# Kernel optimization log

Measured on AMD Instinct MI355X. Metric: run time of the kernel, lower is better.

## Reference

```python
import jax, jax.numpy as jnp
import numpy as np

B, H, S, D = 2, 16, 2048, 64


def setup_inputs() -> dict:
    key = jax.random.key(0)
    k1, k2, k3 = jax.random.split(key, 3)
    qry = jax.random.normal(k1, (B, H, S, D), dtype=jnp.float32)
    k_ = jax.random.normal(k2, (B, H, S, D), dtype=jnp.float32)
    val = jax.random.normal(k3, (B, H, S, D), dtype=jnp.float32)
    # causal mask [B, S_q, S_k]: True = attend, False = masked
    attn_mask = jnp.broadcast_to(jnp.tril(jnp.ones((S, S), dtype=bool)), (B, S, S))
    return {"qry": qry, "key": k_, "val": val, "attn_mask": attn_mask}


def reference(qry, key, val, attn_mask):
    d_k = key.shape[-1]
    # scores: [B, H, S_q, S_k]
    scores = jnp.einsum("bhqd,bhkd->bhqk", qry, key) / jnp.sqrt(jnp.asarray(d_k, qry.dtype))
    if attn_mask is not None:
        # attn_bias: 0 where mask True, -inf where False; broadcast over heads
        bias = jnp.where(attn_mask[:, None, :, :], jnp.asarray(0.0, qry.dtype), jnp.asarray(-jnp.inf, qry.dtype))
        scores = scores + bias
    attn_weights = jax.nn.softmax(scores, axis=-1)
    # dropout_p = 0.0 -> no dropout applied
    output = jnp.einsum("bhqk,bhkd->bhqd", attn_weights, val)
    return (output, attn_weights)
```

## Files before the change

### kernel.cpp

```cpp
#include <hip/hip_runtime.h>

#define NB 2
#define NH 16
#define SEQ 2048
#define HD 64

typedef __attribute__((ext_vector_type(8))) __bf16 bfrag8;
typedef __attribute__((ext_vector_type(4))) __bf16 bvec4;
typedef __attribute__((ext_vector_type(4))) float ffrag4;

#define SCALE2 0.18033688011112042f
#define MASKVAL (-3.0e38f)

__device__ __forceinline__ ffrag4 mfma16(bfrag8 a, bfrag8 b, ffrag4 c) {
    return __builtin_amdgcn_mfma_f32_16x16x32_bf16(a, b, c, 0, 0, 0);
}

__global__ __launch_bounds__(256, 4)
void attn_fwd(const float* __restrict__ Qg, const float* __restrict__ Kg,
              const float* __restrict__ Vg, float* __restrict__ Og,
              float* __restrict__ Pg)
{
    const int bh   = blockIdx.y;
    const int qt   = (blockIdx.x + blockIdx.y) & 31;
    const int q0   = qt * 64;
    const int tid  = threadIdx.x;
    const int wave = tid >> 6;
    const int lane = tid & 63;
    const int l16  = lane & 15;
    const int quad = lane >> 4;

    const float* Qb = Qg + (size_t)bh * SEQ * HD;
    const float* Kb = Kg + (size_t)bh * SEQ * HD;
    const float* Vb = Vg + (size_t)bh * SEQ * HD;
    float* Ob = Og + (size_t)bh * SEQ * HD;
    float* Pb = Pg + (size_t)bh * SEQ * SEQ;

    __shared__ __align__(16) char smem[35840];
    __bf16* Ks  = (__bf16*)smem;
    __bf16* Vts = (__bf16*)(smem + 9216);
    float*  P32 = (float*)(smem + 18432);
    __bf16* Qs  = (__bf16*)(smem + 18432);
    float*  Pw  = P32 + wave * (16 * 68);

    {
        const float4 z4 = make_float4(0.f, 0.f, 0.f, 0.f);
        for (int r = 0; r < 64; ++r) {
            float* dst = Pb + (size_t)(q0 + r) * SEQ;
            for (int c = q0 + 64 + tid * 4; c < SEQ; c += 1024)
                *(float4*)(dst + c) = z4;
        }
    }

    #pragma unroll
    for (int j = 0; j < 4; ++j) {
        int i = tid + 256 * j;
        int row = i >> 4, c4 = (i & 15) * 4;
        float4 v = *(const float4*)(Qb + (size_t)(q0 + row) * HD + c4);
        bvec4 w = { (__bf16)v.x, (__bf16)v.y, (__bf16)v.z, (__bf16)v.w };
        *(bvec4*)&Qs[row * 72 + c4] = w;
    }
    __syncthreads();
    bfrag8 qf0 = *(bfrag8*)&Qs[(wave * 16 + l16) * 72 +  0 + quad * 8];
    bfrag8 qf1 = *(bfrag8*)&Qs[(wave * 16 + l16) * 72 + 32 + quad * 8];

    const int nch   = q0 / 64 + 1;
    const int wrow  = q0 + wave * 16;
    const int myrow = wrow + quad * 4;

    float m_i[4], l_i[4], rl[4];
    #pragma unroll
    for (int r = 0; r < 4; ++r) { m_i[r] = MASKVAL; l_i[r] = 0.f; }

    for (int ch = 0; ch < nch; ++ch) {
        __syncthreads();
        #pragma unroll
        for (int j = 0; j < 4; ++j) {
            int i = tid + 256 * j;
            int row = i >> 4, c4 = (i & 15) * 4;
            float4 v = *(const float4*)(Kb + (size_t)(ch * 64 + row) * HD + c4);
            bvec4 w = { (__bf16)v.x, (__bf16)v.y, (__bf16)v.z, (__bf16)v.w };
            *(bvec4*)&Ks[row * 72 + c4] = w;
        }
        __syncthreads();

        ffrag4 acc[4] = { {0,0,0,0},{0,0,0,0},{0,0,0,0},{0,0,0,0} };
        #pragma unroll
        for (int g = 0; g < 4; ++g) {
            bfrag8 b0 = *(bfrag8*)&Ks[(g * 16 + l16) * 72 + quad * 8];
            bfrag8 b1 = *(bfrag8*)&Ks[(g * 16 + l16) * 72 + 32 + quad * 8];
            acc[g] = mfma16(qf0, b0, acc[g]);
            acc[g] = mfma16(qf1, b1, acc[g]);
        }
        #pragma unroll
        for (int r = 0; r < 4; ++r) {
            const int row = myrow + r;
            float s0 = (ch * 64 +  0 + l16 <= row) ? acc[0][r] * SCALE2 : MASKVAL;
            float s1 = (ch * 64 + 16 + l16 <= row) ? acc[1][r] * SCALE2 : MASKVAL;
            float s2 = (ch * 64 + 32 + l16 <= row) ? acc[2][r] * SCALE2 : MASKVAL;
            float s3 = (ch * 64 + 48 + l16 <= row) ? acc[3][r] * SCALE2 : MASKVAL;
            float mn = fmaxf(fmaxf(s0, s1), fmaxf(s2, s3));
            mn = fmaxf(mn, m_i[r]);
            float e = exp2f(s0 - mn) + exp2f(s1 - mn)
                    + exp2f(s2 - mn) + exp2f(s3 - mn);
            l_i[r] = l_i[r] * exp2f(m_i[r] - mn) + e;
            m_i[r] = mn;
        }
    }

    #pragma unroll
    for (int r = 0; r < 4; ++r) {
        float m = m_i[r], l = l_i[r];
        #pragma unroll
        for (int d = 1; d < 16; d <<= 1) {
            float om = __shfl_xor(m, d, 16);
            float ol = __shfl_xor(l, d, 16);
            float mn = fmaxf(m, om);
            l = l * exp2f(m - mn) + ol * exp2f(om - mn);
            m = mn;
        }
        m_i[r] = m;
        rl[r]  = 1.f / l;
    }

    ffrag4 oacc[4] = { {0,0,0,0},{0,0,0,0},{0,0,0,0},{0,0,0,0} };
    for (int ch = 0; ch < nch; ++ch) {
        __syncthreads();
        #pragma unroll
        for (int j = 0; j < 4; ++j) {
            int i = tid + 256 * j;
            int row = i >> 4, c4 = (i & 15) * 4;
            float4 v = *(const float4*)(Kb + (size_t)(ch * 64 + row) * HD + c4);
            bvec4 w = { (__bf16)v.x, (__bf16)v.y, (__bf16)v.z, (__bf16)v.w };
            *(bvec4*)&Ks[row * 72 + c4] = w;
        }
        #pragma unroll
        for (int j = 0; j < 4; ++j) {
            int i = tid + 256 * j;
            int kk = i >> 4, c4 = (i & 15) * 4;
            float4 v = *(const float4*)(Vb + (size_t)(ch * 64 + kk) * HD + c4);
            Vts[(c4 + 0) * 72 + kk] = (__bf16)v.x;
            Vts[(c4 + 1) * 72 + kk] = (__bf16)v.y;
            Vts[(c4 + 2) * 72 + kk] = (__bf16)v.z;
            Vts[(c4 + 3) * 72 + kk] = (__bf16)v.w;
        }
        __syncthreads();

        ffrag4 acc[4] = { {0,0,0,0},{0,0,0,0},{0,0,0,0},{0,0,0,0} };
        #pragma unroll
        for (int g = 0; g < 4; ++g) {
            bfrag8 b0 = *(bfrag8*)&Ks[(g * 16 + l16) * 72 + quad * 8];
            bfrag8 b1 = *(bfrag8*)&Ks[(g * 16 + l16) * 72 + 32 + quad * 8];
            acc[g] = mfma16(qf0, b0, acc[g]);
            acc[g] = mfma16(qf1, b1, acc[g]);
        }
        #pragma unroll
        for (int r = 0; r < 4; ++r) {
            const int row = myrow + r;
            #pragma unroll
            for (int g = 0; g < 4; ++g) {
                int col = ch * 64 + g * 16 + l16;
                float p = (col <= row)
                        ? exp2f(acc[g][r] * SCALE2 - m_i[r]) * rl[r] : 0.f;
                Pw[(quad * 4 + r) * 68 + g * 16 + l16] = p;
            }
        }
        asm volatile("s_waitcnt lgkmcnt(0)" ::: "memory");

        #pragma unroll
        for (int t = 0; t < 4; ++t) {
            int row = (lane >> 4) + t * 4;
            float4 v = *(float4*)&Pw[row * 68 + (lane & 15) * 4];
            *(float4*)(Pb + (size_t)(wrow + row) * SEQ + ch * 64 + (lane & 15) * 4) = v;
        }

        #pragma unroll
        for (int h = 0; h < 2; ++h) {
            float4 p0 = *(float4*)&Pw[l16 * 68 + h * 32 + quad * 8];
            float4 p1 = *(float4*)&Pw[l16 * 68 + h * 32 + quad * 8 + 4];
            bfrag8 pa = { (__bf16)p0.x, (__bf16)p0.y, (__bf16)p0.z, (__bf16)p0.w,
                          (__bf16)p1.x, (__bf16)p1.y, (__bf16)p1.z, (__bf16)p1.w };
            #pragma unroll
            for (int t = 0; t < 4; ++t) {
                bfrag8 bv = *(bfrag8*)&Vts[(t * 16 + l16) * 72 + h * 32 + quad * 8];
                oacc[t] = mfma16(pa, bv, oacc[t]);
            }
        }
    }

    #pragma unroll
    for (int t = 0; t < 4; ++t)
        #pragma unroll
        for (int r = 0; r < 4; ++r)
            Ob[(size_t)(myrow + r) * HD + t * 16 + l16] = oacc[t][r];
}

extern "C" void kernel_launch(void* const* d_in, const int* in_sizes, int n_in,
                              void* d_out, int out_size, void* d_ws, size_t ws_size,
                              hipStream_t stream) {
    const float* Qg = (const float*)d_in[0];
    const float* Kg = (const float*)d_in[1];
    const float* Vg = (const float*)d_in[2];
    float* Og = (float*)d_out;
    float* Pg = Og + (size_t)NB * NH * SEQ * HD;
    dim3 grid(SEQ / 64, NB * NH);
    attn_fwd<<<grid, dim3(256), 0, stream>>>(Qg, Kg, Vg, Og, Pg);
}
```

Measured before the change: 714.9 us.

## Pre-convert K and transposed V to bf16 workspace and use nontemporal P stores

Adds a pre-pass kernel that converts K to bf16 and V to a transposed bf16 layout in workspace once per call. The attention kernel then loads half the bytes per tile and skips repeated fp32-to-bf16 conversion and scattered transposing LDS writes across its two passes. Stores of the large attention-weights matrix, including the zero fill, become nontemporal to reduce cache pollution. The cost is an extra kernel launch and a workspace round trip.

```diff
diff --git a/kernel.cpp b/kernel.cpp
--- a/kernel.cpp
+++ b/kernel.cpp
@@ -8,6 +8,7 @@
 typedef __attribute__((ext_vector_type(8))) __bf16 bfrag8;
 typedef __attribute__((ext_vector_type(4))) __bf16 bvec4;
 typedef __attribute__((ext_vector_type(4))) float ffrag4;
+typedef __attribute__((ext_vector_type(4))) float f32x4;
 
 #define SCALE2 0.18033688011112042f
 #define MASKVAL (-3.0e38f)
@@ -16,9 +17,52 @@
     return __builtin_amdgcn_mfma_f32_16x16x32_bf16(a, b, c, 0, 0, 0);
 }
 
+__global__ __launch_bounds__(256)
+void cvt_kv(const float* __restrict__ Kg, const float* __restrict__ Vg,
+            __bf16* __restrict__ Kw, __bf16* __restrict__ Vtw)
+{
+    const int bh = blockIdx.y;
+    const int t0 = blockIdx.x * 64;
+    const int tid = threadIdx.x;
+
+    const float* Kb = Kg + (size_t)bh * SEQ * HD;
+    const float* Vb = Vg + (size_t)bh * SEQ * HD;
+    __bf16* Kwb = Kw  + (size_t)bh * SEQ * HD;
+    __bf16* Vwb = Vtw + (size_t)bh * SEQ * HD;
+
+    #pragma unroll
+    for (int j = 0; j < 4; ++j) {
+        int i = tid + 256 * j;
+        int row = i >> 4, c4 = (i & 15) * 4;
+        float4 v = *(const float4*)(Kb + (size_t)(t0 + row) * HD + c4);
+        bvec4 w = { (__bf16)v.x, (__bf16)v.y, (__bf16)v.z, (__bf16)v.w };
+        *(bvec4*)&Kwb[(size_t)(t0 + row) * HD + c4] = w;
+    }
+
+    __shared__ __align__(16) __bf16 Vs[64 * 72];
+    #pragma unroll
+    for (int j = 0; j < 4; ++j) {
+        int i = tid + 256 * j;
+        int row = i >> 4, c4 = (i & 15) * 4;
+        float4 v = *(const float4*)(Vb + (size_t)(t0 + row) * HD + c4);
+        Vs[(c4 + 0) * 72 + row] = (__bf16)v.x;
+        Vs[(c4 + 1) * 72 + row] = (__bf16)v.y;
+        Vs[(c4 + 2) * 72 + row] = (__bf16)v.z;
+        Vs[(c4 + 3) * 72 + row] = (__bf16)v.w;
+    }
+    __syncthreads();
+    #pragma unroll
+    for (int j = 0; j < 2; ++j) {
+        int i = tid + 256 * j;
+        int d = i >> 3, c8 = (i & 7) * 8;
+        bfrag8 w = *(bfrag8*)&Vs[d * 72 + c8];
+        *(bfrag8*)&Vwb[(size_t)d * SEQ + t0 + c8] = w;
+    }
+}
+
 __global__ __launch_bounds__(256, 4)
-void attn_fwd(const float* __restrict__ Qg, const float* __restrict__ Kg,
-              const float* __restrict__ Vg, float* __restrict__ Og,
+void attn_fwd(const float* __restrict__ Qg, const __bf16* __restrict__ Kw,
+              const __bf16* __restrict__ Vtw, float* __restrict__ Og,
               float* __restrict__ Pg)
 {
     const int bh   = blockIdx.y;
@@ -30,9 +74,9 @@
     const int l16  = lane & 15;
     const int quad = lane >> 4;
 
-    const float* Qb = Qg + (size_t)bh * SEQ * HD;
-    const float* Kb = Kg + (size_t)bh * SEQ * HD;
-    const float* Vb = Vg + (size_t)bh * SEQ * HD;
+    const float*  Qb  = Qg  + (size_t)bh * SEQ * HD;
+    const __bf16* Kwb = Kw  + (size_t)bh * SEQ * HD;
+    const __bf16* Vwb = Vtw + (size_t)bh * SEQ * HD;
     float* Ob = Og + (size_t)bh * SEQ * HD;
     float* Pb = Pg + (size_t)bh * SEQ * SEQ;
 
@@ -44,11 +88,11 @@
     float*  Pw  = P32 + wave * (16 * 68);
 
     {
-        const float4 z4 = make_float4(0.f, 0.f, 0.f, 0.f);
+        const f32x4 z4 = {0.f, 0.f, 0.f, 0.f};
         for (int r = 0; r < 64; ++r) {
             float* dst = Pb + (size_t)(q0 + r) * SEQ;
             for (int c = q0 + 64 + tid * 4; c < SEQ; c += 1024)
-                *(float4*)(dst + c) = z4;
+                __builtin_nontemporal_store(z4, (f32x4*)(dst + c));
         }
     }
 
@@ -75,12 +119,11 @@
     for (int ch = 0; ch < nch; ++ch) {
         __syncthreads();
         #pragma unroll
-        for (int j = 0; j < 4; ++j) {
+        for (int j = 0; j < 2; ++j) {
             int i = tid + 256 * j;
-            int row = i >> 4, c4 = (i & 15) * 4;
-            float4 v = *(const float4*)(Kb + (size_t)(ch * 64 + row) * HD + c4);
-            bvec4 w = { (__bf16)v.x, (__bf16)v.y, (__bf16)v.z, (__bf16)v.w };
-            *(bvec4*)&Ks[row * 72 + c4] = w;
+            int row = i >> 3, c8 = (i & 7) * 8;
+            bfrag8 w = *(const bfrag8*)(Kwb + (size_t)(ch * 64 + row) * HD + c8);
+            *(bfrag8*)&Ks[row * 72 + c8] = w;
         }
         __syncthreads();
 
@@ -127,22 +170,18 @@
     for (int ch = 0; ch < nch; ++ch) {
         __syncthreads();
         #pragma unroll
-        for (int j = 0; j < 4; ++j) {
+        for (int j = 0; j < 2; ++j) {
             int i = tid + 256 * j;
-            int row = i >> 4, c4 = (i & 15) * 4;
-            float4 v = *(const float4*)(Kb + (size_t)(ch * 64 + row) * HD + c4);
-            bvec4 w = { (__bf16)v.x, (__bf16)v.y, (__bf16)v.z, (__bf16)v.w };
-            *(bvec4*)&Ks[row * 72 + c4] = w;
-        }
-        #pragma unroll
-        for (int j = 0; j < 4; ++j) {
+            int row = i >> 3, c8 = (i & 7) * 8;
+            bfrag8 w = *(const bfrag8*)(Kwb + (size_t)(ch * 64 + row) * HD + c8);
+            *(bfrag8*)&Ks[row * 72 + c8] = w;
+        }
+        #pragma unroll
+        for (int j = 0; j < 2; ++j) {
             int i = tid + 256 * j;
-            int kk = i >> 4, c4 = (i & 15) * 4;
-            float4 v = *(const float4*)(Vb + (size_t)(ch * 64 + kk) * HD + c4);
-            Vts[(c4 + 0) * 72 + kk] = (__bf16)v.x;
-            Vts[(c4 + 1) * 72 + kk] = (__bf16)v.y;
-            Vts[(c4 + 2) * 72 + kk] = (__bf16)v.z;
-            Vts[(c4 + 3) * 72 + kk] = (__bf16)v.w;
+            int d = i >> 3, c8 = (i & 7) * 8;
+            bfrag8 w = *(const bfrag8*)(Vwb + (size_t)d * SEQ + ch * 64 + c8);
+            *(bfrag8*)&Vts[d * 72 + c8] = w;
         }
         __syncthreads();
 
@@ -170,8 +209,9 @@
         #pragma unroll
         for (int t = 0; t < 4; ++t) {
             int row = (lane >> 4) + t * 4;
-            float4 v = *(float4*)&Pw[row * 68 + (lane & 15) * 4];
-            *(float4*)(Pb + (size_t)(wrow + row) * SEQ + ch * 64 + (lane & 15) * 4) = v;
+            f32x4 v = *(f32x4*)&Pw[row * 68 + (lane & 15) * 4];
+            __builtin_nontemporal_store(v,
+                (f32x4*)(Pb + (size_t)(wrow + row) * SEQ + ch * 64 + (lane & 15) * 4));
         }
 
         #pragma unroll
@@ -203,6 +243,11 @@
     const float* Vg = (const float*)d_in[2];
     float* Og = (float*)d_out;
     float* Pg = Og + (size_t)NB * NH * SEQ * HD;
+
+    __bf16* Kw  = (__bf16*)d_ws;
+    __bf16* Vtw = Kw + (size_t)NB * NH * SEQ * HD;
+
     dim3 grid(SEQ / 64, NB * NH);
-    attn_fwd<<<grid, dim3(256), 0, stream>>>(Qg, Kg, Vg, Og, Pg);
-}
+    cvt_kv<<<grid, dim3(256), 0, stream>>>(Kg, Vg, Kw, Vtw);
+    attn_fwd<<<grid, dim3(256), 0, stream>>>(Qg, Kw, Vtw, Og, Pg);
+}
```

Measured after the change: 657.9 us. 8.0% less time.
